# Kernel optimization log

Measured on AMD Instinct MI355X. Metric: run time of the kernel, lower is better.

## Reference

```python
import jax, jax.numpy as jnp
import numpy as np

B, S, D, H = 4, 2048, 1024, 16
HS = D // H  # head size = 64


def setup_inputs() -> dict:
    key = jax.random.key(0)
    k1, k2, k3 = jax.random.split(key, 3)
    return {
        "input_data": jax.random.normal(k1, (B, S, D), dtype=jnp.float32),
        "w_qkv": jax.random.normal(k2, (D, 3 * D), dtype=jnp.float32) * (1.0 / np.sqrt(D)),
        "b_qkv": jnp.zeros((3 * D,), dtype=jnp.float32),
        "w_proj": jax.random.normal(k3, (D, D), dtype=jnp.float32) * (1.0 / np.sqrt(D)),
        "b_proj": jnp.zeros((D,), dtype=jnp.float32),
    }


def reference(input_data, w_qkv, b_qkv, w_proj, b_proj):
    b, s, d = input_data.shape
    qkv = input_data @ w_qkv + b_qkv  # [b, s, 3d]
    q, k, v = jnp.split(qkv, 3, axis=-1)
    # [b, h, s, hs]
    q = q.reshape(b, s, H, HS).transpose(0, 2, 1, 3)
    k = k.reshape(b, s, H, HS).transpose(0, 2, 1, 3)
    v = v.reshape(b, s, H, HS).transpose(0, 2, 1, 3)
    # NB: original module scales by 1/sqrt(num_heads), not 1/sqrt(head_size)
    scores = jnp.einsum('bhqd,bhkd->bhqk', q, k) / jnp.sqrt(jnp.float32(H))
    causal = jnp.tril(jnp.ones((s, s), dtype=bool))
    scores = jnp.where(causal[None, None], scores, -jnp.inf)
    weights = jax.nn.softmax(scores, axis=-1)  # dropout p=0.0 -> identity
    out = jnp.einsum('bhqk,bhkd->bhqd', weights, v)
    out = out.transpose(0, 2, 1, 3).reshape(b, s, d)
    return out @ w_proj + b_proj
```

## Files before the change

### kernel.cpp

```cpp
#include <hip/hip_runtime.h>


typedef unsigned short u16;
typedef short bf16x8 __attribute__((ext_vector_type(8)));
typedef unsigned short u16x8 __attribute__((ext_vector_type(8)));
typedef float f32x4 __attribute__((ext_vector_type(4)));
typedef float f32x16 __attribute__((ext_vector_type(16)));

#define S_LEN 2048
#define DMODEL 1024
#define NHEAD 16
#define MROWS 8192

#define SCALE_LOG2E 0.36067376022224085f
#define DEFER_THR 8.0f

__device__ __forceinline__ u16 f2bf(float f) {
  union { float f; unsigned u; } c; c.f = f;
  unsigned u = c.u;
  u += 0x7fffu + ((u >> 16) & 1u);
  return (u16)(u >> 16);
}

__device__ __forceinline__ float exp2_fast(float x) {
  float r; asm("v_exp_f32 %0, %1" : "=v"(r) : "v"(x)); return r;
}

__device__ __forceinline__ unsigned cvtpk_bf16(float a, float b) {
  unsigned r;
  asm("v_cvt_pk_bf16_f32 %0, %1, %2" : "=v"(r) : "v"(a), "v"(b));
  return r;
}

__device__ __forceinline__ void plswap(unsigned& a, unsigned& b) {
  asm("v_permlane32_swap_b32 %0, %1" : "+v"(a), "+v"(b));
}

__device__ __forceinline__ f32x4 mfma16(bf16x8 a, bf16x8 b, f32x4 c) {
  return __builtin_amdgcn_mfma_f32_16x16x32_bf16(a, b, c, 0, 0, 0);
}

__device__ __forceinline__ f32x16 mfma32(bf16x8 a, bf16x8 b, f32x16 c) {
  return __builtin_amdgcn_mfma_f32_32x32x16_bf16(a, b, c, 0, 0, 0);
}

__device__ __forceinline__ void gload_lds16(const void* g, void* l) {
  __builtin_amdgcn_global_load_lds((__attribute__((address_space(1))) void*)g,
                                   (__attribute__((address_space(3))) void*)l,
                                   16, 0, 0);
}

__global__ void k_f32_to_bf16(const float* __restrict__ in, u16* __restrict__ out, int n) {
  int i = (blockIdx.x * 256 + threadIdx.x) * 4;
  if (i < n) {
    float4 v = *reinterpret_cast<const float4*>(in + i);
    ushort4 o;
    o.x = f2bf(v.x); o.y = f2bf(v.y); o.z = f2bf(v.z); o.w = f2bf(v.w);
    *reinterpret_cast<ushort4*>(out + i) = o;
  }
}

__global__ void k_transpose_to_bf16(const float* __restrict__ in, u16* __restrict__ out,
                                    int K, int N) {
  __shared__ float t[32][33];
  int n0 = blockIdx.x * 32, k0 = blockIdx.y * 32;
  int tx = threadIdx.x & 31, ty = threadIdx.x >> 5;
#pragma unroll
  for (int i = 0; i < 32; i += 8)
    t[ty + i][tx] = in[(size_t)(k0 + ty + i) * N + n0 + tx];
  __syncthreads();
#pragma unroll
  for (int i = 0; i < 32; i += 8)
    out[(size_t)(n0 + ty + i) * K + k0 + tx] = f2bf(t[tx][ty + i]);
}

template <int MODE>
__global__ __launch_bounds__(512, 1) void k_gemm8(const u16* __restrict__ A,
                                                  const u16* __restrict__ Bt,
                                                  const float* __restrict__ bias,
                                                  u16* __restrict__ outb,
                                                  float* __restrict__ outf,
                                                  u16* __restrict__ vtout,
                                                  int N, int K) {
  __shared__ u16 As[2][2][256 * 32];
  __shared__ u16 Bs[2][2][128 * 32];

  const int tid = threadIdx.x;
  const int lane = tid & 63, wave = tid >> 6;
  const int wr = wave >> 1, wc = wave & 1;
  const int lr = lane & 15, lk = lane >> 4;
  const int m0 = blockIdx.x * 256, n0 = blockIdx.y * 128;
  const size_t Kb = (size_t)K * 2;

  const int csw = ((tid & 3) ^ ((tid >> 3) & 3)) * 16;
  const char* Asrc0 = (const char*)A + (size_t)(m0 + (tid >> 2)) * Kb + csw;
  const char* Asrc1 = Asrc0 + 128 * Kb;
  const char* Bsrc0 = (const char*)Bt + (size_t)(n0 + (tid >> 2)) * Kb + csw;

#define STAGE_KH(BUFX, KH, T)                                                  \
  {                                                                            \
    const size_t ko_ = (size_t)(T) * 128 + (KH) * 64;                          \
    gload_lds16(Asrc0 + ko_, &As[BUFX][KH][(size_t)tid * 8]);                  \
    gload_lds16(Asrc1 + ko_, &As[BUFX][KH][((size_t)tid + 512) * 8]);          \
    gload_lds16(Bsrc0 + ko_, &Bs[BUFX][KH][(size_t)tid * 8]);                  \
  }

  f32x4 zero4 = {0.f, 0.f, 0.f, 0.f};
  f32x4 acc[4][4];
#pragma unroll
  for (int m = 0; m < 4; ++m)
#pragma unroll
    for (int n = 0; n < 4; ++n) acc[m][n] = zero4;

  const int slotsw = (lr >> 1) & 3;

#define PHASE(BUFX, KH, T, DOSTAGE, VMZERO)                                    \
  {                                                                            \
    if (VMZERO) asm volatile("s_waitcnt vmcnt(0)" ::: "memory");               \
    else        asm volatile("s_waitcnt vmcnt(3)" ::: "memory");               \
    __builtin_amdgcn_s_barrier();                                              \
    __builtin_amdgcn_sched_barrier(0);                                         \
    bf16x8 af[4], bfr[4];                                                      \
    _Pragma("unroll") for (int m = 0; m < 4; ++m)                              \
        af[m] = *reinterpret_cast<const bf16x8*>(                              \
            &As[BUFX][KH][(wr * 64 + m * 16 + lr) * 32 + ((lk ^ slotsw) * 8)]);\
    _Pragma("unroll") for (int n = 0; n < 4; ++n)                              \
        bfr[n] = *reinterpret_cast<const bf16x8*>(                             \
            &Bs[BUFX][KH][(wc * 64 + n * 16 + lr) * 32 + ((lk ^ slotsw) * 8)]);\
    if (DOSTAGE) STAGE_KH((BUFX) ^ 1, KH, (T) + 1);                            \
    __builtin_amdgcn_sched_barrier(0);                                         \
    __builtin_amdgcn_s_setprio(1);                                             \
    _Pragma("unroll") for (int m = 0; m < 4; ++m)                              \
        _Pragma("unroll") for (int n = 0; n < 4; ++n)                          \
            acc[m][n] = mfma16(af[m], bfr[n], acc[m][n]);                      \
    __builtin_amdgcn_s_setprio(0);                                             \
  }

  const int nkt = K >> 6;
  STAGE_KH(0, 0, 0);
  STAGE_KH(0, 1, 0);

  for (int t = 0; t < nkt - 1; ++t) {
    const int buf = t & 1;
    PHASE(buf, 0, t, 1, 0);
    PHASE(buf, 1, t, 1, 0);
  }
  {
    const int buf = (nkt - 1) & 1;
    PHASE(buf, 0, nkt - 1, 0, 0);
    PHASE(buf, 1, nkt - 1, 0, 1);
  }
#undef PHASE
#undef STAGE_KH

#pragma unroll
  for (int n = 0; n < 4; ++n) {
    int col = n0 + wc * 64 + n * 16 + lr;
    float bv = bias[col];
#pragma unroll
    for (int m = 0; m < 4; ++m) {
      int rowb = m0 + wr * 64 + m * 16 + lk * 4;
      if (MODE == 1) {
#pragma unroll
        for (int r = 0; r < 4; ++r)
          outf[(size_t)(rowb + r) * N + col] = acc[m][n][r] + bv;
      } else {
        if (col < 2048) {
#pragma unroll
          for (int r = 0; r < 4; ++r)
            outb[(size_t)(rowb + r) * 2048 + col] = f2bf(acc[m][n][r] + bv);
        } else {
          int hh = (col >> 6) & 15, dd = col & 63;
          int bb = rowb >> 11, ss = rowb & 2047;
          ushort4 o;
          o.x = f2bf(acc[m][n][0] + bv);
          o.y = f2bf(acc[m][n][1] + bv);
          o.z = f2bf(acc[m][n][2] + bv);
          o.w = f2bf(acc[m][n][3] + bv);
          *reinterpret_cast<ushort4*>(
              vtout + ((size_t)(bb * 16 + hh) * 64 + dd) * 2048 + ss) = o;
        }
      }
    }
  }
}

__global__ __launch_bounds__(256, 2) void k_attn5(const u16* __restrict__ qk,
                                                  const u16* __restrict__ vt,
                                                  u16* __restrict__ ao) {
  __shared__ u16 Ks[2][4096];
  __shared__ u16 Vs[2][4096];

  const int tid = threadIdx.x;
  const int lane = tid & 63, wave = tid >> 6;
  const int l31 = lane & 31, hi = lane >> 5;
  const int gid = blockIdx.x;
  const int bh = gid & 63;
  const int tq = gid >> 6;
  const int qb = (tq < 4) ? tq : 11 - tq;
  const int b = bh >> 4, h = bh & 15;

  const int qlo0 = qb * 128 + wave * 32;
  const int qhi0 = 1920 - qb * 128 + wave * 32;
  const int ktd_lo = qlo0 >> 6;
  const int ktd_hi = qhi0 >> 6;
  const int KTMAX = 31 - 2 * qb;
  const int qrel0 = qlo0 + l31 - ktd_lo * 64;
  const int qrel1 = qhi0 + l31 - ktd_hi * 64;

  bf16x8 qf[2][4];
  {
    const u16* q0p = qk + ((size_t)b * S_LEN + qlo0 + l31) * 2048 + h * 64 + hi * 8;
    const u16* q1p = qk + ((size_t)b * S_LEN + qhi0 + l31) * 2048 + h * 64 + hi * 8;
#pragma unroll
    for (int ks = 0; ks < 4; ++ks) {
      qf[0][ks] = *reinterpret_cast<const bf16x8*>(q0p + ks * 16);
      qf[1][ks] = *reinterpret_cast<const bf16x8*>(q1p + ks * 16);
    }
  }

  const int swzcol = 16 * ((lane & 7) ^ (lane >> 3));
  const char* kg = (const char*)qk + ((size_t)b * S_LEN) * 4096 + 2048 + h * 128 +
                   (size_t)(lane >> 3) * 4096 + swzcol;
  const char* vg = (const char*)vt + ((size_t)bh * 64 + (lane >> 3)) * 4096 + swzcol;

#define STAGE(BUF, KT)                                                              \
  {                                                                                 \
    const char* kg_ = kg + (size_t)(KT) * 64 * 4096;                                \
    const char* vg_ = vg + (size_t)(KT) * 128;                                      \
    gload_lds16(kg_ + (size_t)(wave * 8) * 4096, &Ks[BUF][wave * 512]);             \
    gload_lds16(kg_ + (size_t)((wave + 4) * 8) * 4096, &Ks[BUF][(wave + 4) * 512]); \
    gload_lds16(vg_ + (size_t)(wave * 8) * 4096, &Vs[BUF][wave * 512]);             \
    gload_lds16(vg_ + (size_t)((wave + 4) * 8) * 4096, &Vs[BUF][(wave + 4) * 512]); \
  }

  f32x16 oT[2][2];
#pragma unroll
  for (int m = 0; m < 2; ++m)
#pragma unroll
    for (int kb = 0; kb < 2; ++kb)
#pragma unroll
      for (int g = 0; g < 16; ++g) oT[m][kb][g] = 0.f;
  float m_i[2] = {-INFINITY, -INFINITY};
  float l_i[2] = {0.f, 0.f};

  const int rsw = (l31 & 7) << 4;

#define SM32(SC, M, MASKED, QREL, FR)                                           \
  {                                                                             \
    float s_[2][16];                                                            \
    float mx_ = -INFINITY;                                                      \
    _Pragma("unroll") for (int kb = 0; kb < 2; ++kb)                            \
      _Pragma("unroll") for (int g = 0; g < 16; ++g) {                          \
        float v_ = SC[kb][g] * SCALE_LOG2E;                                     \
        if (MASKED) {                                                           \
          int key_ = kb * 32 + (g & 3) + ((g >> 2) << 3) + hi * 4;              \
          if (key_ > (QREL)) v_ = -INFINITY;                                    \
        }                                                                       \
        s_[kb][g] = v_;                                                         \
        mx_ = fmaxf(mx_, v_);                                                   \
      }                                                                         \
    mx_ = fmaxf(mx_, __shfl_xor(mx_, 32, 64));                                  \
    if (__any(mx_ > m_i[M] + DEFER_THR)) {                                      \
      float mn_ = fmaxf(m_i[M], mx_);                                           \
      float c_ = exp2_fast(m_i[M] - mn_);                                       \
      m_i[M] = mn_;                                                             \
      l_i[M] *= c_;                                                             \
      _Pragma("unroll") for (int kb = 0; kb < 2; ++kb)                          \
        _Pragma("unroll") for (int g = 0; g < 16; ++g) oT[M][kb][g] *= c_;      \
    }                                                                           \
    float rs_ = 0.f;                                                            \
    unsigned pk_[8][2];                                                         \
    _Pragma("unroll") for (int kb = 0; kb < 2; ++kb)                            \
      _Pragma("unroll") for (int s = 0; s < 4; ++s) {                           \
        float p0_ = exp2_fast(s_[kb][s * 4 + 0] - m_i[M]);                      \
        float p1_ = exp2_fast(s_[kb][s * 4 + 1] - m_i[M]);                      \
        float p2_ = exp2_fast(s_[kb][s * 4 + 2] - m_i[M]);                      \
        float p3_ = exp2_fast(s_[kb][s * 4 + 3] - m_i[M]);                      \
        rs_ += (p0_ + p1_) + (p2_ + p3_);                                       \
        pk_[kb * 4 + s][0] = cvtpk_bf16(p0_, p1_);                              \
        pk_[kb * 4 + s][1] = cvtpk_bf16(p2_, p3_);                              \
      }                                                                         \
    rs_ += __shfl_xor(rs_, 32, 64);                                             \
    l_i[M] += rs_;                                                              \
    _Pragma("unroll") for (int t = 0; t < 4; ++t) {                             \
      unsigned a0_ = pk_[2 * t][0], b0_ = pk_[2 * t + 1][0];                    \
      unsigned a1_ = pk_[2 * t][1], b1_ = pk_[2 * t + 1][1];                    \
      plswap(a0_, b0_);                                                         \
      plswap(a1_, b1_);                                                         \
      FR[t][0] = a0_; FR[t][1] = a1_; FR[t][2] = b0_; FR[t][3] = b1_;           \
    }                                                                           \
  }

  STAGE(0, 0);
  __syncthreads();
  int buf = 0;

  for (int kt = 0; kt <= KTMAX; ++kt) {
    if (kt < KTMAX) STAGE(buf ^ 1, kt + 1);

    const char* Kb = (const char*)&Ks[buf][0];
    const char* Vb = (const char*)&Vs[buf][0];
    const bool lo_act = (kt <= ktd_lo);
    const bool hi_act = (kt <= ktd_hi);
    const bool mask0 = (kt == ktd_lo), mask1 = (kt == ktd_hi);

    bf16x8 kf[2][4];
#pragma unroll
    for (int kb = 0; kb < 2; ++kb)
#pragma unroll
      for (int ks = 0; ks < 4; ++ks)
        kf[kb][ks] = *reinterpret_cast<const bf16x8*>(
            Kb + (kb * 32 + l31) * 128 + ((ks * 32 + hi * 16) ^ rsw));

    f32x16 sc0[2], sc1[2];
#pragma unroll
    for (int kb = 0; kb < 2; ++kb) {
      if (hi_act) {
        sc1[kb] = mfma32(kf[kb][0], qf[1][0], f32x16{});
#pragma unroll
        for (int ks = 1; ks < 4; ++ks) sc1[kb] = mfma32(kf[kb][ks], qf[1][ks], sc1[kb]);
      }
      if (lo_act) {
        sc0[kb] = mfma32(kf[kb][0], qf[0][0], f32x16{});
#pragma unroll
        for (int ks = 1; ks < 4; ++ks) sc0[kb] = mfma32(kf[kb][ks], qf[0][ks], sc0[kb]);
      }
    }

    bf16x8 vf[2][4];
#pragma unroll
    for (int kbd = 0; kbd < 2; ++kbd)
#pragma unroll
      for (int t = 0; t < 4; ++t)
        vf[kbd][t] = *reinterpret_cast<const bf16x8*>(
            Vb + (kbd * 32 + l31) * 128 + ((t * 32 + hi * 16) ^ rsw));

    if (lo_act) {
      unsigned fr0[4][4];
      SM32(sc0, 0, mask0, qrel0, fr0);
#pragma unroll
      for (int t = 0; t < 4; ++t) {
        bf16x8 pb = *reinterpret_cast<const bf16x8*>(&fr0[t][0]);
        oT[0][0] = mfma32(vf[0][t], pb, oT[0][0]);
        oT[0][1] = mfma32(vf[1][t], pb, oT[0][1]);
      }
    }
    if (hi_act) {
      unsigned fr1[4][4];
      SM32(sc1, 1, mask1, qrel1, fr1);
#pragma unroll
      for (int t = 0; t < 4; ++t) {
        bf16x8 pb = *reinterpret_cast<const bf16x8*>(&fr1[t][0]);
        oT[1][0] = mfma32(vf[0][t], pb, oT[1][0]);
        oT[1][1] = mfma32(vf[1][t], pb, oT[1][1]);
      }
    }

    __syncthreads();
    buf ^= 1;
  }
#undef SM32
#undef STAGE

#pragma unroll
  for (int m = 0; m < 2; ++m) {
    const int qbase = (m == 0) ? qlo0 : qhi0;
    float inv = 1.f / l_i[m];
    u16* orow = ao + ((size_t)b * S_LEN + qbase + l31) * DMODEL + h * 64 + hi * 4;
#pragma unroll
    for (int kbd = 0; kbd < 2; ++kbd)
#pragma unroll
      for (int s = 0; s < 4; ++s) {
        unsigned w0 = cvtpk_bf16(oT[m][kbd][s * 4 + 0] * inv, oT[m][kbd][s * 4 + 1] * inv);
        unsigned w1 = cvtpk_bf16(oT[m][kbd][s * 4 + 2] * inv, oT[m][kbd][s * 4 + 3] * inv);
        *reinterpret_cast<unsigned*>(orow + kbd * 32 + s * 8) = w0;
        *reinterpret_cast<unsigned*>(orow + kbd * 32 + s * 8 + 2) = w1;
      }
  }
}

extern "C" void kernel_launch(void* const* d_in, const int* in_sizes, int n_in,
                              void* d_out, int out_size, void* d_ws, size_t ws_size,
                              hipStream_t stream) {
  const float* x = (const float*)d_in[0];
  const float* wqkv = (const float*)d_in[1];
  const float* bqkv = (const float*)d_in[2];
  const float* wproj = (const float*)d_in[3];
  const float* bproj = (const float*)d_in[4];
  float* out = (float*)d_out;

  char* ws = (char*)d_ws;
  u16* Xb     = (u16*)(ws);
  u16* Wqkvt  = (u16*)(ws + (size_t)16777216);
  u16* Wprojt = (u16*)(ws + (size_t)23068672);
  u16* QKb    = (u16*)(ws + (size_t)25165824);
  u16* Vt     = (u16*)(ws + (size_t)58720256);
  u16* AOb    = (u16*)(ws + (size_t)75497472);

  k_f32_to_bf16<<<MROWS * DMODEL / 4 / 256, 256, 0, stream>>>(x, Xb, MROWS * DMODEL);
  k_transpose_to_bf16<<<dim3(3072 / 32, 1024 / 32), 256, 0, stream>>>(wqkv, Wqkvt, 1024, 3072);
  k_transpose_to_bf16<<<dim3(1024 / 32, 1024 / 32), 256, 0, stream>>>(wproj, Wprojt, 1024, 1024);

  k_gemm8<2><<<dim3(MROWS / 256, 3072 / 128), 512, 0, stream>>>(
      Xb, Wqkvt, bqkv, QKb, nullptr, Vt, 3072, 1024);

  k_attn5<<<dim3(512), 256, 0, stream>>>(QKb, Vt, AOb);

  k_gemm8<1><<<dim3(MROWS / 256, DMODEL / 128), 512, 0, stream>>>(
      AOb, Wprojt, bproj, nullptr, out, nullptr, DMODEL, 1024);
}
```

Baseline: 184.8 us.

## Split paired-query attention blocks into single tiles and fold score scale into Q

The attention kernel previously paired a low and a high query tile in each block to balance causal work. It now gives each block one 128-row query tile, doubles the grid to 1024 blocks and raises the occupancy hint to 4 blocks per CU. Tiles are ordered so heavy and light tiles interleave across the launch. The softmax scale times log2(e) is folded into Q in the QKV GEMM epilogue, which removes a multiply per score, and the row max and row sum now use four independent accumulators to shorten dependency chains. The cost is loading each K/V tile separately for each query tile instead of sharing it between a pair, and relying on the scheduler to balance uneven causal work.

```diff
diff --git a/kernel.cpp b/kernel.cpp
--- a/kernel.cpp
+++ b/kernel.cpp
@@ -166,9 +166,10 @@
           outf[(size_t)(rowb + r) * N + col] = acc[m][n][r] + bv;
       } else {
         if (col < 2048) {
+          const float qs = (col < 1024) ? SCALE_LOG2E : 1.0f;
 #pragma unroll
           for (int r = 0; r < 4; ++r)
-            outb[(size_t)(rowb + r) * 2048 + col] = f2bf(acc[m][n][r] + bv);
+            outb[(size_t)(rowb + r) * 2048 + col] = f2bf((acc[m][n][r] + bv) * qs);
         } else {
           int hh = (col >> 6) & 15, dd = col & 63;
           int bb = rowb >> 11, ss = rowb & 2047;
@@ -185,7 +186,7 @@
   }
 }
 
-__global__ __launch_bounds__(256, 2) void k_attn5(const u16* __restrict__ qk,
+__global__ __launch_bounds__(256, 4) void k_attn6(const u16* __restrict__ qk,
                                                   const u16* __restrict__ vt,
                                                   u16* __restrict__ ao) {
   __shared__ u16 Ks[2][4096];
@@ -197,26 +198,24 @@
   const int gid = blockIdx.x;
   const int bh = gid & 63;
   const int tq = gid >> 6;
-  const int qb = (tq < 4) ? tq : 11 - tq;
+  const int g2 = tq >> 2, r2 = tq & 3;
+  const int qt = (g2 == 0) ? 2 * r2
+               : (g2 == 1) ? 15 - 2 * r2
+               : (g2 == 2) ? 2 * r2 + 1
+                           : 14 - 2 * r2;
   const int b = bh >> 4, h = bh & 15;
 
-  const int qlo0 = qb * 128 + wave * 32;
-  const int qhi0 = 1920 - qb * 128 + wave * 32;
-  const int ktd_lo = qlo0 >> 6;
-  const int ktd_hi = qhi0 >> 6;
-  const int KTMAX = 31 - 2 * qb;
-  const int qrel0 = qlo0 + l31 - ktd_lo * 64;
-  const int qrel1 = qhi0 + l31 - ktd_hi * 64;
-
-  bf16x8 qf[2][4];
+  const int q0 = qt * 128 + wave * 32;
+  const int ktd = (q0 + 31) >> 6;
+  const int KTMAX = 2 * qt + 1;
+  const int qrel = q0 + l31 - ktd * 64;
+
+  bf16x8 qf[4];
   {
-    const u16* q0p = qk + ((size_t)b * S_LEN + qlo0 + l31) * 2048 + h * 64 + hi * 8;
-    const u16* q1p = qk + ((size_t)b * S_LEN + qhi0 + l31) * 2048 + h * 64 + hi * 8;
-#pragma unroll
-    for (int ks = 0; ks < 4; ++ks) {
-      qf[0][ks] = *reinterpret_cast<const bf16x8*>(q0p + ks * 16);
-      qf[1][ks] = *reinterpret_cast<const bf16x8*>(q1p + ks * 16);
-    }
+    const u16* qp = qk + ((size_t)b * S_LEN + q0 + l31) * 2048 + h * 64 + hi * 8;
+#pragma unroll
+    for (int ks = 0; ks < 4; ++ks)
+      qf[ks] = *reinterpret_cast<const bf16x8*>(qp + ks * 16);
   }
 
   const int swzcol = 16 * ((lane & 7) ^ (lane >> 3));
@@ -234,63 +233,15 @@
     gload_lds16(vg_ + (size_t)((wave + 4) * 8) * 4096, &Vs[BUF][(wave + 4) * 512]); \
   }
 
-  f32x16 oT[2][2];
-#pragma unroll
-  for (int m = 0; m < 2; ++m)
-#pragma unroll
-    for (int kb = 0; kb < 2; ++kb)
-#pragma unroll
-      for (int g = 0; g < 16; ++g) oT[m][kb][g] = 0.f;
-  float m_i[2] = {-INFINITY, -INFINITY};
-  float l_i[2] = {0.f, 0.f};
+  f32x16 oT[2];
+#pragma unroll
+  for (int kb = 0; kb < 2; ++kb)
+#pragma unroll
+    for (int g = 0; g < 16; ++g) oT[kb][g] = 0.f;
+  float m_i = -INFINITY;
+  float l_i = 0.f;
 
   const int rsw = (l31 & 7) << 4;
-
-#define SM32(SC, M, MASKED, QREL, FR)                                           \
-  {                                                                             \
-    float s_[2][16];                                                            \
-    float mx_ = -INFINITY;                                                      \
-    _Pragma("unroll") for (int kb = 0; kb < 2; ++kb)                            \
-      _Pragma("unroll") for (int g = 0; g < 16; ++g) {                          \
-        float v_ = SC[kb][g] * SCALE_LOG2E;                                     \
-        if (MASKED) {                                                           \
-          int key_ = kb * 32 + (g & 3) + ((g >> 2) << 3) + hi * 4;              \
-          if (key_ > (QREL)) v_ = -INFINITY;                                    \
-        }                                                                       \
-        s_[kb][g] = v_;                                                         \
-        mx_ = fmaxf(mx_, v_);                                                   \
-      }                                                                         \
-    mx_ = fmaxf(mx_, __shfl_xor(mx_, 32, 64));                                  \
-    if (__any(mx_ > m_i[M] + DEFER_THR)) {                                      \
-      float mn_ = fmaxf(m_i[M], mx_);                                           \
-      float c_ = exp2_fast(m_i[M] - mn_);                                       \
-      m_i[M] = mn_;                                                             \
-      l_i[M] *= c_;                                                             \
-      _Pragma("unroll") for (int kb = 0; kb < 2; ++kb)                          \
-        _Pragma("unroll") for (int g = 0; g < 16; ++g) oT[M][kb][g] *= c_;      \
-    }                                                                           \
-    float rs_ = 0.f;                                                            \
-    unsigned pk_[8][2];                                                         \
-    _Pragma("unroll") for (int kb = 0; kb < 2; ++kb)                            \
-      _Pragma("unroll") for (int s = 0; s < 4; ++s) {                           \
-        float p0_ = exp2_fast(s_[kb][s * 4 + 0] - m_i[M]);                      \
-        float p1_ = exp2_fast(s_[kb][s * 4 + 1] - m_i[M]);                      \
-        float p2_ = exp2_fast(s_[kb][s * 4 + 2] - m_i[M]);                      \
-        float p3_ = exp2_fast(s_[kb][s * 4 + 3] - m_i[M]);                      \
-        rs_ += (p0_ + p1_) + (p2_ + p3_);                                       \
-        pk_[kb * 4 + s][0] = cvtpk_bf16(p0_, p1_);                              \
-        pk_[kb * 4 + s][1] = cvtpk_bf16(p2_, p3_);                              \
-      }                                                                         \
-    rs_ += __shfl_xor(rs_, 32, 64);                                             \
-    l_i[M] += rs_;                                                              \
-    _Pragma("unroll") for (int t = 0; t < 4; ++t) {                             \
-      unsigned a0_ = pk_[2 * t][0], b0_ = pk_[2 * t + 1][0];                    \
-      unsigned a1_ = pk_[2 * t][1], b1_ = pk_[2 * t + 1][1];                    \
-      plswap(a0_, b0_);                                                         \
-      plswap(a1_, b1_);                                                         \
-      FR[t][0] = a0_; FR[t][1] = a1_; FR[t][2] = b0_; FR[t][3] = b1_;           \
-    }                                                                           \
-  }
 
   STAGE(0, 0);
   __syncthreads();
@@ -299,81 +250,118 @@
   for (int kt = 0; kt <= KTMAX; ++kt) {
     if (kt < KTMAX) STAGE(buf ^ 1, kt + 1);
 
-    const char* Kb = (const char*)&Ks[buf][0];
-    const char* Vb = (const char*)&Vs[buf][0];
-    const bool lo_act = (kt <= ktd_lo);
-    const bool hi_act = (kt <= ktd_hi);
-    const bool mask0 = (kt == ktd_lo), mask1 = (kt == ktd_hi);
-
-    bf16x8 kf[2][4];
-#pragma unroll
-    for (int kb = 0; kb < 2; ++kb)
-#pragma unroll
-      for (int ks = 0; ks < 4; ++ks)
-        kf[kb][ks] = *reinterpret_cast<const bf16x8*>(
-            Kb + (kb * 32 + l31) * 128 + ((ks * 32 + hi * 16) ^ rsw));
-
-    f32x16 sc0[2], sc1[2];
-#pragma unroll
-    for (int kb = 0; kb < 2; ++kb) {
-      if (hi_act) {
-        sc1[kb] = mfma32(kf[kb][0], qf[1][0], f32x16{});
-#pragma unroll
-        for (int ks = 1; ks < 4; ++ks) sc1[kb] = mfma32(kf[kb][ks], qf[1][ks], sc1[kb]);
-      }
-      if (lo_act) {
-        sc0[kb] = mfma32(kf[kb][0], qf[0][0], f32x16{});
-#pragma unroll
-        for (int ks = 1; ks < 4; ++ks) sc0[kb] = mfma32(kf[kb][ks], qf[0][ks], sc0[kb]);
-      }
-    }
-
-    bf16x8 vf[2][4];
-#pragma unroll
-    for (int kbd = 0; kbd < 2; ++kbd)
-#pragma unroll
-      for (int t = 0; t < 4; ++t)
-        vf[kbd][t] = *reinterpret_cast<const bf16x8*>(
-            Vb + (kbd * 32 + l31) * 128 + ((t * 32 + hi * 16) ^ rsw));
-
-    if (lo_act) {
-      unsigned fr0[4][4];
-      SM32(sc0, 0, mask0, qrel0, fr0);
+    if (kt <= ktd) {
+      const char* Kb = (const char*)&Ks[buf][0];
+      const char* Vb = (const char*)&Vs[buf][0];
+      const bool masked = (kt == ktd);
+
+      bf16x8 kf[2][4];
+#pragma unroll
+      for (int kb = 0; kb < 2; ++kb)
+#pragma unroll
+        for (int ks = 0; ks < 4; ++ks)
+          kf[kb][ks] = *reinterpret_cast<const bf16x8*>(
+              Kb + (kb * 32 + l31) * 128 + ((ks * 32 + hi * 16) ^ rsw));
+
+      f32x16 sc[2];
+#pragma unroll
+      for (int kb = 0; kb < 2; ++kb) {
+        sc[kb] = mfma32(kf[kb][0], qf[0], f32x16{});
+#pragma unroll
+        for (int ks = 1; ks < 4; ++ks) sc[kb] = mfma32(kf[kb][ks], qf[ks], sc[kb]);
+      }
+
+      bf16x8 vf[2][4];
+#pragma unroll
+      for (int kbd = 0; kbd < 2; ++kbd)
+#pragma unroll
+        for (int t = 0; t < 4; ++t)
+          vf[kbd][t] = *reinterpret_cast<const bf16x8*>(
+              Vb + (kbd * 32 + l31) * 128 + ((t * 32 + hi * 16) ^ rsw));
+
+      if (masked) {
+#pragma unroll
+        for (int kb = 0; kb < 2; ++kb)
+#pragma unroll
+          for (int g = 0; g < 16; ++g) {
+            int key_ = kb * 32 + (g & 3) + ((g >> 2) << 3) + hi * 4;
+            if (key_ > qrel) sc[kb][g] = -INFINITY;
+          }
+      }
+      float mxa = fmaxf(sc[0][0], sc[0][4]), mxb = fmaxf(sc[0][1], sc[0][5]);
+      float mxc = fmaxf(sc[0][2], sc[0][6]), mxd = fmaxf(sc[0][3], sc[0][7]);
+#pragma unroll
+      for (int g = 8; g < 16; g += 4) {
+        mxa = fmaxf(mxa, sc[0][g]);     mxb = fmaxf(mxb, sc[0][g + 1]);
+        mxc = fmaxf(mxc, sc[0][g + 2]); mxd = fmaxf(mxd, sc[0][g + 3]);
+      }
+#pragma unroll
+      for (int g = 0; g < 16; g += 4) {
+        mxa = fmaxf(mxa, sc[1][g]);     mxb = fmaxf(mxb, sc[1][g + 1]);
+        mxc = fmaxf(mxc, sc[1][g + 2]); mxd = fmaxf(mxd, sc[1][g + 3]);
+      }
+      float mx = fmaxf(fmaxf(mxa, mxb), fmaxf(mxc, mxd));
+      mx = fmaxf(mx, __shfl_xor(mx, 32, 64));
+      if (__any(mx > m_i + DEFER_THR)) {
+        float mn = fmaxf(m_i, mx);
+        float c = exp2_fast(m_i - mn);
+        m_i = mn;
+        l_i *= c;
+#pragma unroll
+        for (int kb = 0; kb < 2; ++kb)
+#pragma unroll
+          for (int g = 0; g < 16; ++g) oT[kb][g] *= c;
+      }
+      float rsa = 0.f, rsb = 0.f, rsc = 0.f, rsd = 0.f;
+      unsigned pk_[8][2];
+#pragma unroll
+      for (int kb = 0; kb < 2; ++kb)
+#pragma unroll
+        for (int s = 0; s < 4; ++s) {
+          float p0 = exp2_fast(sc[kb][s * 4 + 0] - m_i);
+          float p1 = exp2_fast(sc[kb][s * 4 + 1] - m_i);
+          float p2 = exp2_fast(sc[kb][s * 4 + 2] - m_i);
+          float p3 = exp2_fast(sc[kb][s * 4 + 3] - m_i);
+          rsa += p0; rsb += p1; rsc += p2; rsd += p3;
+          pk_[kb * 4 + s][0] = cvtpk_bf16(p0, p1);
+          pk_[kb * 4 + s][1] = cvtpk_bf16(p2, p3);
+        }
+      float rs = (rsa + rsb) + (rsc + rsd);
+      rs += __shfl_xor(rs, 32, 64);
+      l_i += rs;
+
+      bf16x8 pfr[4];
 #pragma unroll
       for (int t = 0; t < 4; ++t) {
-        bf16x8 pb = *reinterpret_cast<const bf16x8*>(&fr0[t][0]);
-        oT[0][0] = mfma32(vf[0][t], pb, oT[0][0]);
-        oT[0][1] = mfma32(vf[1][t], pb, oT[0][1]);
-      }
-    }
-    if (hi_act) {
-      unsigned fr1[4][4];
-      SM32(sc1, 1, mask1, qrel1, fr1);
+        unsigned a0 = pk_[2 * t][0], b0 = pk_[2 * t + 1][0];
+        unsigned a1 = pk_[2 * t][1], b1 = pk_[2 * t + 1][1];
+        plswap(a0, b0);
+        plswap(a1, b1);
+        unsigned fr[4] = {a0, a1, b0, b1};
+        pfr[t] = *reinterpret_cast<const bf16x8*>(&fr[0]);
+      }
+
 #pragma unroll
       for (int t = 0; t < 4; ++t) {
-        bf16x8 pb = *reinterpret_cast<const bf16x8*>(&fr1[t][0]);
-        oT[1][0] = mfma32(vf[0][t], pb, oT[1][0]);
-        oT[1][1] = mfma32(vf[1][t], pb, oT[1][1]);
+        oT[0] = mfma32(vf[0][t], pfr[t], oT[0]);
+        oT[1] = mfma32(vf[1][t], pfr[t], oT[1]);
       }
     }
 
     __syncthreads();
     buf ^= 1;
   }
-#undef SM32
 #undef STAGE
 
-#pragma unroll
-  for (int m = 0; m < 2; ++m) {
-    const int qbase = (m == 0) ? qlo0 : qhi0;
-    float inv = 1.f / l_i[m];
-    u16* orow = ao + ((size_t)b * S_LEN + qbase + l31) * DMODEL + h * 64 + hi * 4;
+  {
+    float inv = 1.f / l_i;
+    u16* orow = ao + ((size_t)b * S_LEN + q0 + l31) * DMODEL + h * 64 + hi * 4;
 #pragma unroll
     for (int kbd = 0; kbd < 2; ++kbd)
 #pragma unroll
       for (int s = 0; s < 4; ++s) {
-        unsigned w0 = cvtpk_bf16(oT[m][kbd][s * 4 + 0] * inv, oT[m][kbd][s * 4 + 1] * inv);
-        unsigned w1 = cvtpk_bf16(oT[m][kbd][s * 4 + 2] * inv, oT[m][kbd][s * 4 + 3] * inv);
+        unsigned w0 = cvtpk_bf16(oT[kbd][s * 4 + 0] * inv, oT[kbd][s * 4 + 1] * inv);
+        unsigned w1 = cvtpk_bf16(oT[kbd][s * 4 + 2] * inv, oT[kbd][s * 4 + 3] * inv);
         *reinterpret_cast<unsigned*>(orow + kbd * 32 + s * 8) = w0;
         *reinterpret_cast<unsigned*>(orow + kbd * 32 + s * 8 + 2) = w1;
       }
@@ -405,7 +393,7 @@
   k_gemm8<2><<<dim3(MROWS / 256, 3072 / 128), 512, 0, stream>>>(
       Xb, Wqkvt, bqkv, QKb, nullptr, Vt, 3072, 1024);
 
-  k_attn5<<<dim3(512), 256, 0, stream>>>(QKb, Vt, AOb);
+  k_attn6<<<dim3(1024), 256, 0, stream>>>(QKb, Vt, AOb);
 
   k_gemm8<1><<<dim3(MROWS / 256, DMODEL / 128), 512, 0, stream>>>(
       AOb, Wprojt, bproj, nullptr, out, nullptr, DMODEL, 1024);
```

Measured after the change: 191.6 us. +3.7%, slower.

## Triple-buffer GEMM K-loop, fold softmax scale into Q, add MFMA priority

Applied to the files above, without the earlier changes.

The GEMM moves from double to triple buffering in shared memory, prefetching two K-tiles ahead, and adjusts the vmcnt waits so global loads overlap more compute. The softmax scale (times log2 e) is applied to Q when the QKV GEMM writes it out, which removes a multiply per score in the attention kernel at the cost of rounding the scaled Q to bf16. The attention kernel also raises wave priority around its MFMA blocks. Triple buffering raises LDS use per block, and a wrong vmcnt count could cause stale reads.

```diff
diff --git a/kernel.cpp b/kernel.cpp
--- a/kernel.cpp
+++ b/kernel.cpp
@@ -14,6 +14,9 @@
 
 #define SCALE_LOG2E 0.36067376022224085f
 #define DEFER_THR 8.0f
+
+#define WAITVM_(N) asm volatile("s_waitcnt vmcnt(" #N ")" ::: "memory")
+#define WAITVM(N) WAITVM_(N)
 
 __device__ __forceinline__ u16 f2bf(float f) {
   union { float f; unsigned u; } c; c.f = f;
@@ -82,8 +85,8 @@
                                                   float* __restrict__ outf,
                                                   u16* __restrict__ vtout,
                                                   int N, int K) {
-  __shared__ u16 As[2][2][256 * 32];
-  __shared__ u16 Bs[2][2][128 * 32];
+  __shared__ u16 As[3][2][256 * 32];
+  __shared__ u16 Bs[3][2][128 * 32];
 
   const int tid = threadIdx.x;
   const int lane = tid & 63, wave = tid >> 6;
@@ -114,10 +117,9 @@
 
   const int slotsw = (lr >> 1) & 3;
 
-#define PHASE(BUFX, KH, T, DOSTAGE, VMZERO)                                    \
+#define PHASE(BUFX, KH, VM, DOSTAGE, SBUF, ST)                                 \
   {                                                                            \
-    if (VMZERO) asm volatile("s_waitcnt vmcnt(0)" ::: "memory");               \
-    else        asm volatile("s_waitcnt vmcnt(3)" ::: "memory");               \
+    WAITVM(VM);                                                                \
     __builtin_amdgcn_s_barrier();                                              \
     __builtin_amdgcn_sched_barrier(0);                                         \
     bf16x8 af[4], bfr[4];                                                      \
@@ -127,7 +129,7 @@
     _Pragma("unroll") for (int n = 0; n < 4; ++n)                              \
         bfr[n] = *reinterpret_cast<const bf16x8*>(                             \
             &Bs[BUFX][KH][(wc * 64 + n * 16 + lr) * 32 + ((lk ^ slotsw) * 8)]);\
-    if (DOSTAGE) STAGE_KH((BUFX) ^ 1, KH, (T) + 1);                            \
+    if (DOSTAGE) STAGE_KH(SBUF, KH, ST);                                       \
     __builtin_amdgcn_sched_barrier(0);                                         \
     __builtin_amdgcn_s_setprio(1);                                             \
     _Pragma("unroll") for (int m = 0; m < 4; ++m)                              \
@@ -139,16 +141,24 @@
   const int nkt = K >> 6;
   STAGE_KH(0, 0, 0);
   STAGE_KH(0, 1, 0);
-
-  for (int t = 0; t < nkt - 1; ++t) {
-    const int buf = t & 1;
-    PHASE(buf, 0, t, 1, 0);
-    PHASE(buf, 1, t, 1, 0);
+  STAGE_KH(1, 0, 1);
+  STAGE_KH(1, 1, 1);
+
+  for (int t = 0; t < nkt - 2; ++t) {
+    const int bf3 = t % 3;
+    const int bn3 = (t + 2) % 3;
+    PHASE(bf3, 0, 6, 1, bn3, t + 2);
+    PHASE(bf3, 1, 9, 1, bn3, t + 2);
   }
   {
-    const int buf = (nkt - 1) & 1;
-    PHASE(buf, 0, nkt - 1, 0, 0);
-    PHASE(buf, 1, nkt - 1, 0, 1);
+    const int bf3 = (nkt - 2) % 3;
+    PHASE(bf3, 0, 6, 0, 0, 0);
+    PHASE(bf3, 1, 6, 0, 0, 0);
+  }
+  {
+    const int bf3 = (nkt - 1) % 3;
+    PHASE(bf3, 0, 0, 0, 0, 0);
+    PHASE(bf3, 1, 0, 0, 0, 0);
   }
 #undef PHASE
 #undef STAGE_KH
@@ -166,9 +176,10 @@
           outf[(size_t)(rowb + r) * N + col] = acc[m][n][r] + bv;
       } else {
         if (col < 2048) {
+          const float qs = (col < 1024) ? SCALE_LOG2E : 1.0f;
 #pragma unroll
           for (int r = 0; r < 4; ++r)
-            outb[(size_t)(rowb + r) * 2048 + col] = f2bf(acc[m][n][r] + bv);
+            outb[(size_t)(rowb + r) * 2048 + col] = f2bf((acc[m][n][r] + bv) * qs);
         } else {
           int hh = (col >> 6) & 15, dd = col & 63;
           int bb = rowb >> 11, ss = rowb & 2047;
@@ -185,9 +196,9 @@
   }
 }
 
-__global__ __launch_bounds__(256, 2) void k_attn5(const u16* __restrict__ qk,
-                                                  const u16* __restrict__ vt,
-                                                  u16* __restrict__ ao) {
+__global__ __launch_bounds__(256, 2) void k_attn13(const u16* __restrict__ qk,
+                                                   const u16* __restrict__ vt,
+                                                   u16* __restrict__ ao) {
   __shared__ u16 Ks[2][4096];
   __shared__ u16 Vs[2][4096];
 
@@ -252,7 +263,7 @@
     float mx_ = -INFINITY;                                                      \
     _Pragma("unroll") for (int kb = 0; kb < 2; ++kb)                            \
       _Pragma("unroll") for (int g = 0; g < 16; ++g) {                          \
-        float v_ = SC[kb][g] * SCALE_LOG2E;                                     \
+        float v_ = SC[kb][g];                                                   \
         if (MASKED) {                                                           \
           int key_ = kb * 32 + (g & 3) + ((g >> 2) << 3) + hi * 4;              \
           if (key_ > (QREL)) v_ = -INFINITY;                                    \
@@ -314,6 +325,7 @@
             Kb + (kb * 32 + l31) * 128 + ((ks * 32 + hi * 16) ^ rsw));
 
     f32x16 sc0[2], sc1[2];
+    __builtin_amdgcn_s_setprio(1);
 #pragma unroll
     for (int kb = 0; kb < 2; ++kb) {
       if (hi_act) {
@@ -327,6 +339,7 @@
         for (int ks = 1; ks < 4; ++ks) sc0[kb] = mfma32(kf[kb][ks], qf[0][ks], sc0[kb]);
       }
     }
+    __builtin_amdgcn_s_setprio(0);
 
     bf16x8 vf[2][4];
 #pragma unroll
@@ -339,22 +352,26 @@
     if (lo_act) {
       unsigned fr0[4][4];
       SM32(sc0, 0, mask0, qrel0, fr0);
+      __builtin_amdgcn_s_setprio(1);
 #pragma unroll
       for (int t = 0; t < 4; ++t) {
         bf16x8 pb = *reinterpret_cast<const bf16x8*>(&fr0[t][0]);
         oT[0][0] = mfma32(vf[0][t], pb, oT[0][0]);
         oT[0][1] = mfma32(vf[1][t], pb, oT[0][1]);
       }
+      __builtin_amdgcn_s_setprio(0);
     }
     if (hi_act) {
       unsigned fr1[4][4];
       SM32(sc1, 1, mask1, qrel1, fr1);
+      __builtin_amdgcn_s_setprio(1);
 #pragma unroll
       for (int t = 0; t < 4; ++t) {
         bf16x8 pb = *reinterpret_cast<const bf16x8*>(&fr1[t][0]);
         oT[1][0] = mfma32(vf[0][t], pb, oT[1][0]);
         oT[1][1] = mfma32(vf[1][t], pb, oT[1][1]);
       }
+      __builtin_amdgcn_s_setprio(0);
     }
 
     __syncthreads();
@@ -405,7 +422,7 @@
   k_gemm8<2><<<dim3(MROWS / 256, 3072 / 128), 512, 0, stream>>>(
       Xb, Wqkvt, bqkv, QKb, nullptr, Vt, 3072, 1024);
 
-  k_attn5<<<dim3(512), 256, 0, stream>>>(QKb, Vt, AOb);
+  k_attn13<<<dim3(512), 256, 0, stream>>>(QKb, Vt, AOb);
 
   k_gemm8<1><<<dim3(MROWS / 256, DMODEL / 128), 512, 0, stream>>>(
       AOb, Wprojt, bproj, nullptr, out, nullptr, DMODEL, 1024);
```

Result: no change. 181.3 us (-1.9%).
